# Kernel tuning notes

Hardware: AMD Instinct MI355X
Metric: run time of the kernel (lower is better)

The kernel has to match this reference:

```python
import jax, jax.numpy as jnp
import numpy as np

ALPHA = 200.0      # cfg.TRAIN.VOTING_ALPHA
RHO = 100.0        # ADMM penalty
SIGMA = 1e-3       # ADMM regularization
ITERS = 150        # fixed ADMM iterations


def _admm_qp(Q, q, C, l, u):
    n = Q.shape[0]
    K = Q + SIGMA * jnp.eye(n, dtype=Q.dtype) + RHO * (C.T @ C)
    cf = jax.scipy.linalg.cho_factor(K)
    x0 = jnp.zeros((n,), Q.dtype)
    z0 = jnp.clip(jnp.zeros((C.shape[0],), Q.dtype), l, u)
    y0 = jnp.zeros((C.shape[0],), Q.dtype)

    def step(carry, _):
        x, z, y = carry
        rhs = SIGMA * x - q + C.T @ (RHO * z - y)
        x = jax.scipy.linalg.cho_solve(cf, rhs)
        Cx = C @ x
        z = jnp.clip(Cx + y / RHO, l, u)
        y = y + RHO * (Cx - z)
        return (x, z, y), None

    (x, _, _), _ = jax.lax.scan(step, (x0, z0, y0), None, length=ITERS)
    return x


def _l2n(x, axis):
    return x / jnp.maximum(jnp.linalg.norm(x, axis=axis, keepdims=True), 1e-12)


def _forward(feat_tra, feat_det, iou_mat, W, b):
    n1, d = feat_tra.shape
    n2 = feat_det.shape[0]
    # cross-graph feature update
    Mp0 = feat_tra @ feat_det.T + iou_mat                      # (n1,n2)
    m1 = Mp0 @ feat_det                                        # (n1,d)
    m2 = Mp0.T @ feat_tra                                      # (n2,d)
    lam1 = jax.lax.stop_gradient(jnp.linalg.norm(feat_tra, axis=1, keepdims=True)
                                 / jnp.linalg.norm(m1, axis=1, keepdims=True))
    lam2 = jax.lax.stop_gradient(jnp.linalg.norm(feat_det, axis=1, keepdims=True)
                                 / jnp.linalg.norm(m2, axis=1, keepdims=True))
    e1 = jax.nn.relu((feat_tra + lam1 * m1) @ W.T + b)
    e2 = jax.nn.relu((feat_det + lam2 * m2) @ W.T + b)
    e1 = _l2n(e1, 1)
    e2 = _l2n(e2, 1)
    Mp = e1 @ e2.T                                             # (n1,n2) unary affinity
    P = Mp.T                                                   # (n2,n1)
    # Quadratic affinity: the torch code builds src_tgt[i,j,k,l] = <cat(e1_i,e1_j), cat(e2_k,e2_l)>
    # = Mp[i,k] + Mp[j,l], then gathers M[(a,c),(b,d)] = src_tgt[c,d,a,b]/2 masked by (a!=b)&(c!=d).
    ms = 1.0 - jnp.eye(n1, dtype=Mp.dtype)
    mt = 1.0 - jnp.eye(n2, dtype=Mp.dtype)
    M4 = 0.5 * (P[:, :, None, None] + P[None, None, :, :]) \
         * (mt[:, None, :, None] * ms[None, :, None, :])       # (n2,n1,n2,n1)
    n = n1 * n2
    Q = float((n1 - 1) * (n2 - 1)) * jnp.eye(n, dtype=Mp.dtype) - M4.reshape(n, n)
    q = -P.reshape(-1)                                         # -Mpp
    # equality constraints (square case): column sums and row sums == 1
    A = jnp.concatenate([jnp.kron(jnp.ones((1, n1)), jnp.eye(n2)),
                         jnp.kron(jnp.eye(n1), jnp.ones((1, n2)))], axis=0).astype(Mp.dtype)
    C = jnp.concatenate([jnp.eye(n, dtype=Mp.dtype), A], axis=0)
    l = jnp.concatenate([jnp.zeros((n,), Mp.dtype), jnp.ones((n1 + n2,), Mp.dtype)])
    u = jnp.concatenate([jnp.full((n,), 1e6, Mp.dtype), jnp.ones((n1 + n2,), Mp.dtype)])
    x = _admm_qp(Q, q, C, l, u)
    s = x.reshape(n2, n1).T                                    # (n1,n2)
    s = jnp.clip(s, 0.0, 1.0)                                  # relu(s) - relu(s-1)
    s = jax.nn.softmax(ALPHA * s, axis=-1)                     # Voting layer
    return s[None]                                             # (1,n1,n2)


def setup_inputs() -> dict:
    key = jax.random.key(0)
    k1, k2, k3, k4 = jax.random.split(key, 4)
    n1 = n2 = 64
    d = 512
    feat_tra = jax.random.normal(k1, (n1, d), jnp.float32)
    feat_det = jax.random.normal(k2, (n2, d), jnp.float32)
    iou_mat = jax.random.uniform(k3, (n1, n2), jnp.float32)
    W = jnp.eye(d, dtype=jnp.float32) + 0.01 * jax.random.normal(k4, (d, d), jnp.float32)
    b = jnp.zeros((d,), jnp.float32)
    return {"feat_tra": feat_tra, "feat_det": feat_det, "iou_mat": iou_mat, "W": W, "b": b}


def reference(feat_tra, feat_det, iou_mat, W, b):
    return _forward(feat_tra, feat_det, iou_mat, W, b)
```

## Files before the change

### kernel.cpp

```cpp
#include <hip/hip_runtime.h>
#include <math.h>

#define DD 512
#define NS 258
#define NSP 264
#define NWG 64
#define BLK 1024
#define RHO_ 100.0
#define SIG_ 1e-3
#define NITER 150
#define DELTA0 (3969.0 + SIG_ + RHO_)

typedef float v2f __attribute__((ext_vector_type(2)));

#define OFF_E1     512u
#define OFF_SUMS   512u
#define OFF_INV    4608u
#define OFF_E2     262656u
#define OFF_P      524800u
#define OFF_W      557568u
#define OFF_P32    590336u
#define OFF_W32    606720u
#define OFF_KSA    623104u
#define OFF_KSB    1168000u
#define OFF_N32    1712896u

__device__ __forceinline__ int perm258(int i){
  return (i < 128) ? i : (i == 128) ? 256 : (i == 129) ? 257 : (i - 2);
}

template<int CTRL>
__device__ __forceinline__ float dppadd(float v){
  int t = __builtin_amdgcn_mov_dpp(__float_as_int(v), CTRL, 0xF, 0xF, 1);
  return v + __int_as_float(t);
}
template<int CTRL>
__device__ __forceinline__ float dppmax(float v){
  int t = __builtin_amdgcn_mov_dpp(__float_as_int(v), CTRL, 0xF, 0xF, 1);
  return fmaxf(v, __int_as_float(t));
}
__device__ __forceinline__ float sum16(float v){
  v = dppadd<0xB1>(v);
  v = dppadd<0x4E>(v);
  v = dppadd<0x124>(v);
  v = dppadd<0x128>(v);
  return v;
}
__device__ __forceinline__ float wsum64f(float v){
  v = sum16(v);
  v += __shfl_xor(v, 16, 64);
  v += __shfl_xor(v, 32, 64);
  return v;
}
__device__ __forceinline__ float wsum64u(float v){
  v = sum16(v);
  v = dppadd<0x142>(v);
  v = dppadd<0x143>(v);
  return __uint_as_float(__builtin_amdgcn_readlane(__float_as_uint(v), 63));
}
__device__ __forceinline__ float wmax64f(float v){
  v = dppmax<0xB1>(v); v = dppmax<0x4E>(v); v = dppmax<0x124>(v); v = dppmax<0x128>(v);
  v = fmaxf(v, __shfl_xor(v, 16, 64));
  v = fmaxf(v, __shfl_xor(v, 32, 64));
  return v;
}

__device__ __forceinline__ double gsum16d(double v){
  v += __shfl_xor(v, 1, 64);
  v += __shfl_xor(v, 2, 64);
  v += __shfl_xor(v, 4, 64);
  v += __shfl_xor(v, 8, 64);
  return v;
}
__device__ __forceinline__ double wsum64d(double v){
  v = gsum16d(v);
  v += __shfl_xor(v, 16, 64);
  v += __shfl_xor(v, 32, 64);
  return v;
}

__device__ __forceinline__ void decode_idx(int t, int& cls, int& pr, int& ix){
  if (t < 64)       { cls = 1; pr = 1; ix = t; }
  else if (t < 128) { cls = 2; pr = 1; ix = t - 64; }
  else if (t == 128){ cls = 0; pr = 1; ix = 0; }
  else if (t == 129){ cls = 0; pr = 0; ix = 0; }
  else if (t < 194) { cls = 1; pr = 0; ix = t - 130; }
  else              { cls = 2; pr = 0; ix = t - 194; }
}

__device__ __forceinline__ double ksval(int r, int c, const double* __restrict__ p,
                                        const double* __restrict__ w, const double* sumsL){
  int cr, prr, ir, cc, prc, ic;
  decode_idx(r, cr, prr, ir);
  decode_idx(c, cc, prc, ic);
  int m = prr + prc;
  double tval;
  if (cr == 0 && cc == 0)      tval = sumsL[m];
  else if (cr == 0 && cc == 1) tval = sumsL[8 + m*64 + ic];
  else if (cr == 1 && cc == 0) tval = sumsL[8 + m*64 + ir];
  else if (cr == 0 && cc == 2) tval = sumsL[200 + m*64 + ic];
  else if (cr == 2 && cc == 0) tval = sumsL[200 + m*64 + ir];
  else if (cr == 1 && cc == 1) tval = (ir == ic) ? sumsL[8 + m*64 + ir] : 0.0;
  else if (cr == 2 && cc == 2) tval = (ir == ic) ? sumsL[200 + m*64 + ir] : 0.0;
  else if (cr == 1 && cc == 2){
    double wv = w[ic*64 + ir], pv = p[ic*64 + ir];
    tval = (m == 0) ? wv : (m == 1) ? wv*pv : wv*pv*pv;
  } else {
    double wv = w[ir*64 + ic], pv = p[ir*64 + ic];
    tval = (m == 0) ? wv : (m == 1) ? wv*pv : wv*pv*pv;
  }
  double mv2 = 0.0;
  if (cr == 0 && cc == 0 && prr != prc) mv2 = -2.0;
  if (cr != 0 && cr == cc && ir == ic){
    if (prr != prc) mv2 = 2.0;
    else if (prr == 1) mv2 = -4.0 * RHO_;
  }
  return tval + mv2;
}

__global__ __launch_bounds__(BLK) void kp_feat(const float* __restrict__ ft,
                                               const float* __restrict__ fd,
                                               const float* __restrict__ iou,
                                               const float* __restrict__ Wm,
                                               const float* __restrict__ bb,
                                               char* ws){
  double* e1 = (double*)(ws + OFF_E1);
  double* e2 = (double*)(ws + OFF_E2);
  __shared__ double SH[2216];
  const int tid  = threadIdx.x;
  const int wg   = blockIdx.x;
  const int lane = tid & 63;
  const int wv   = tid >> 6;
  float* ftR = (float*)SH;
  float* fdR = ftR + 512;
  float* u1R = fdR + 512;
  float* u2R = u1R + 512;
  double* m0r = SH + 1024;
  double* m0c = m0r + 64;
  double* wp  = m0c + 64;
  double* sca = wp + 32;
  double* vbuf = SH + 1192;
  const int i = wg;
  if (tid < 512){ ftR[tid] = ft[i*DD + tid]; fdR[tid] = fd[i*DD + tid]; }
  {
    double nf = 0.0, nd = 0.0;
    if (tid < 512){
      float a = ftR[tid], b = fdR[tid];
      nf = (double)a*a; nd = (double)b*b;
    }
    nf = wsum64d(nf); nd = wsum64d(nd);
    if (lane == 0){ wp[wv] = nf; wp[16 + wv] = nd; }
    __syncthreads();
    if (tid == 0){
      double s0 = 0, s1 = 0;
      for (int q = 0; q < 16; ++q){ s0 += wp[q]; s1 += wp[16+q]; }
      sca[0] = s0; sca[1] = s1;
    }
  }
  {
    int j = tid >> 4, sub = tid & 15;
    double ar = 0.0, ac = 0.0;
    for (int t2 = 0; t2 < 32; ++t2){
      int k = t2*16 + sub;
      ar += (double)ftR[k] * (double)fd[(size_t)j*DD + k];
      ac += (double)fdR[k] * (double)ft[(size_t)j*DD + k];
    }
    ar = gsum16d(ar); ac = gsum16d(ac);
    if (sub == 0){
      m0r[j] = ar + (double)iou[i*64 + j];
      m0c[j] = ac + (double)iou[j*64 + i];
    }
  }
  __syncthreads();
  {
    int c = tid & 511, half = tid >> 9;
    const double* m0 = half ? m0c : m0r;
    const float*  FB = half ? ft  : fd;
    double a0 = 0, b0 = 0, c0 = 0, d0 = 0;
    for (int a2 = 0; a2 < 64; a2 += 4){
      a0 += m0[a2]   * (double)FB[(size_t)(a2  )*DD + c];
      b0 += m0[a2+1] * (double)FB[(size_t)(a2+1)*DD + c];
      c0 += m0[a2+2] * (double)FB[(size_t)(a2+2)*DD + c];
      d0 += m0[a2+3] * (double)FB[(size_t)(a2+3)*DD + c];
    }
    double mv = (a0 + b0) + (c0 + d0);
    double nn = wsum64d(mv*mv);
    if (lane == 0) wp[wv] = nn;
    __syncthreads();
    if (tid < 2){
      double s = 0;
      for (int q = tid*8; q < tid*8 + 8; ++q) s += wp[q];
      sca[2 + tid] = sqrt(sca[tid] / s);
    }
    __syncthreads();
    double l = sca[2 + half];
    float* uR = half ? u2R : u1R;
    const float* fR = half ? fdR : ftR;
    uR[c] = (float)((double)fR[c] + l*mv);
  }
  __syncthreads();
  {
    const int g16 = tid >> 4;
    const int sub = tid & 15;
    for (int pass = 0; pass < 16; ++pass){
      int c_all = pass*64 + g16;
      int c = c_all & 511, half = c_all >> 9;
      const float* uR  = half ? u2R : u1R;
      const float* wrp = Wm + (size_t)c*DD;
      double acc = 0.0;
#pragma unroll
      for (int j = 0; j < 8; ++j){
        int k = sub*4 + j*64;
        float4 wq = *(const float4*)(wrp + k);
        float4 uq = *(const float4*)(uR + k);
        acc += (double)uq.x*wq.x + (double)uq.y*wq.y + (double)uq.z*wq.z + (double)uq.w*wq.w;
      }
      acc = gsum16d(acc);
      if (sub == 0) vbuf[c_all] = fmax(acc + (double)bb[c], 0.0);
    }
    __syncthreads();
    double v = vbuf[tid];
    double nn = wsum64d(v*v);
    if (lane == 0) wp[wv] = nn;
    __syncthreads();
    if (tid < 2){
      double s = 0;
      for (int q = tid*8; q < tid*8 + 8; ++q) s += wp[q];
      sca[4 + tid] = 1.0 / fmax(sqrt(s), 1e-12);
    }
    __syncthreads();
    int c = tid & 511, half = tid >> 9;
    double* e = half ? e2 : e1;
    e[(size_t)i*DD + c] = v * sca[4 + half];
  }
}

__global__ __launch_bounds__(BLK) void kp_pw(char* ws){
  const double* e1 = (const double*)(ws + OFF_E1);
  const double* e2 = (const double*)(ws + OFF_E2);
  double* p   = (double*)(ws + OFF_P);
  double* w   = (double*)(ws + OFF_W);
  float*  p32 = (float*) (ws + OFF_P32);
  float*  w32 = (float*) (ws + OFF_W32);
  __shared__ double e2R[512];
  const int tid = threadIdx.x;
  const int a = blockIdx.x;
  if (tid < 512) e2R[tid] = e2[(size_t)a*DD + tid];
  __syncthreads();
  int b = tid >> 4, sub = tid & 15;
  double a0 = 0.0, a1 = 0.0;
  for (int t2 = 0; t2 < 32; t2 += 2){
    a0 += e1[(size_t)b*DD + t2*16 + sub]     * e2R[t2*16 + sub];
    a1 += e1[(size_t)b*DD + (t2+1)*16 + sub] * e2R[(t2+1)*16 + sub];
  }
  double acc = gsum16d(a0 + a1);
  if (sub == 0){
    double pv = acc;
    double wv2 = 1.0 / (DELTA0 - pv);
    int jj = a*64 + b;
    p[jj] = pv; w[jj] = wv2; p32[jj] = (float)pv; w32[jj] = (float)wv2;
  }
}

__global__ __launch_bounds__(BLK) void kp_sums(char* ws){
  const double* p = (const double*)(ws + OFF_P);
  const double* w = (const double*)(ws + OFF_W);
  double* sumsG = (double*)(ws + OFF_SUMS);
  __shared__ double sumsL[456];
  const int tid = threadIdx.x;
  int a = tid >> 4, sub = tid & 15;
  {
    double r0 = 0, r1 = 0, r2 = 0;
    for (int b = sub*4; b < sub*4 + 4; ++b){
      double wv = w[a*64 + b], pv = p[a*64 + b];
      r0 += wv; r1 += wv*pv; r2 += wv*pv*pv;
    }
    r0 = gsum16d(r0); r1 = gsum16d(r1); r2 = gsum16d(r2);
    if (sub == 0){ sumsL[200 + a] = r0; sumsL[264 + a] = r1; sumsL[328 + a] = r2; }
  }
  {
    int b2 = tid >> 4;
    double c0 = 0, c1 = 0, c2 = 0;
    for (int a2 = sub*4; a2 < sub*4 + 4; ++a2){
      double wv = w[a2*64 + b2], pv = p[a2*64 + b2];
      c0 += wv; c1 += wv*pv; c2 += wv*pv*pv;
    }
    c0 = gsum16d(c0); c1 = gsum16d(c1); c2 = gsum16d(c2);
    if (sub == 0){ sumsL[8 + b2] = c0; sumsL[72 + b2] = c1; sumsL[136 + b2] = c2; }
  }
  __syncthreads();
  if (tid == 0){
    double t0 = 0, t1 = 0, t2 = 0;
    for (int a3 = 0; a3 < 64; ++a3){
      t0 += sumsL[200 + a3]; t1 += sumsL[264 + a3]; t2 += sumsL[328 + a3];
    }
    sumsL[0] = t0; sumsL[1] = t1; sumsL[2] = t2;
    sumsL[3] = 0; sumsL[4] = 0; sumsL[5] = 0; sumsL[6] = 0; sumsL[7] = 0;
  }
  if (tid >= 64 && tid < 128){
    int k = tid - 64;
    sumsL[392 + k] = 1.0 / (sumsL[136 + k] - 4.0*RHO_);
  }
  __syncthreads();
  for (int idx = tid; idx < 456; idx += BLK) sumsG[idx] = sumsL[idx];
}

__global__ __launch_bounds__(BLK) void kp_p3(char* ws){
  const double* p = (const double*)(ws + OFF_P);
  const double* w = (const double*)(ws + OFF_W);
  const double* sumsG = (const double*)(ws + OFF_SUMS);
  double* KsB = (double*)(ws + OFF_KSB);
  __shared__ double sumsL[456];
  __shared__ double temp[68];
  const int tid = threadIdx.x;
  const int c = blockIdx.x;
  for (int idx = tid; idx < 456; idx += BLK) sumsL[idx] = sumsG[idx];
  __syncthreads();
  const double* invd = sumsL + 392;
  if (tid < 64){
    int k = tid;
    temp[k] = (c < 64) ? ((k == c) ? invd[k] : 0.0) : ksval(k, c, p, w, sumsL) * invd[k];
  }
  __syncthreads();
  const double* tp = temp;
  const int s = tid & 3;
  auto dorow = [&](int rr){
    if (rr < 64){
      if (s == 0) KsB[(size_t)rr*NSP + c] = tp[rr];
      return;
    }
    double acc = 0.0;
    if (rr < 128){
      const double* wr_ = w + (rr-64)*64;
      const double* pr_ = p + (rr-64)*64;
      for (int k = s; k < 64; k += 4){ double pv = pr_[k]; acc += wr_[k]*pv*pv*tp[k]; }
    } else if (rr == 128){
      for (int k = s; k < 64; k += 4) acc += sumsL[136 + k]*tp[k];
    } else if (rr == 129){
      for (int k = s; k < 64; k += 4) acc += sumsL[72 + k]*tp[k];
    } else if (rr < 194){
      if (s == 0){ int ir = rr - 130; acc = (sumsL[72 + ir] + 2.0)*tp[ir]; }
    } else {
      int ir = rr - 194;
      const double* wr_ = w + ir*64;
      const double* pr_ = p + ir*64;
      for (int k = s; k < 64; k += 4) acc += wr_[k]*pr_[k]*tp[k];
    }
    acc += __shfl_xor(acc, 1, 64);
    acc += __shfl_xor(acc, 2, 64);
    if (s == 0){
      double first = (c < 64) ? 0.0 : ksval(rr, c, p, w, sumsL);
      KsB[(size_t)rr*NSP + c] = first - acc;
    }
  };
  { int r = tid >> 2; if (r < 256) dorow(r); }
  if (tid < 8) dorow(256 + (tid >> 2));
}

template<int MM>
__global__ __launch_bounds__(BLK) void kp_inv(const double* __restrict__ src, int p0,
                                              double* __restrict__ invG){
  __shared__ double M[MM*67];
  __shared__ double RV[MM], RV2[MM], CV[MM], CV2[MM];
  const int tid = threadIdx.x;
  const int lane = tid & 63, wv = tid >> 6;
  for (int idx = tid; idx < MM*MM; idx += BLK)
    M[(idx/MM)*67 + (idx%MM)] = src[(size_t)(p0 + idx/MM)*NSP + p0 + idx%MM];
  __syncthreads();
  for (int k = 0; k < MM; k += 2){
    if (tid < MM){
      int j = tid;
      double pk  = 1.0 / M[k*67 + k];
      double ck1 = M[(k+1)*67 + k];
      double rv  = M[k*67 + j] * pk;
      if (j == k) rv += pk;
      double rk1 = M[k*67 + k+1] * pk;
      double q   = 1.0 / (M[(k+1)*67 + k+1] - ck1*rk1);
      double r2  = (M[(k+1)*67 + j] - ck1*rv) * q;
      if (j == k+1) r2 += q;
      RV[j] = rv; RV2[j] = r2;
    } else if (tid >= 512 && tid < 512 + MM){
      int i = tid - 512;
      double pk  = 1.0 / M[k*67 + k];
      double rk1 = M[k*67 + k+1] * pk;
      double cv  = M[i*67 + k];
      if (i == k) cv -= 1.0;
      double c2  = M[i*67 + k+1] - cv*rk1;
      if (i == k+1) c2 -= 1.0;
      CV[i] = cv; CV2[i] = c2;
    }
    __syncthreads();
    {
      double rv0 = RV[lane], rv20 = RV2[lane];
      const bool hi = (lane + 64) < MM;
      double rv1 = hi ? RV[lane + 64] : 0.0;
      double rv21 = hi ? RV2[lane + 64] : 0.0;
      for (int i = wv; i < MM; i += 16){
        double cv = CV[i], c2 = CV2[i];
        M[i*67 + lane] -= cv*rv0 + c2*rv20;
        if (hi) M[i*67 + lane + 64] -= cv*rv1 + c2*rv21;
      }
    }
    __syncthreads();
  }
  for (int idx = tid; idx < MM*MM; idx += BLK)
    invG[(idx/MM)*67 + idx%MM] = M[(idx/MM)*67 + idx%MM];
}

template<int MM>
__global__ __launch_bounds__(BLK) void kp_apply(const double* __restrict__ src,
                                                double* __restrict__ dstD,
                                                float* __restrict__ dstF, int p0,
                                                const double* __restrict__ invG){
  __shared__ double M[4422];
  __shared__ double temp[68];
  __shared__ double srcMid[66];
  const int tid = threadIdx.x;
  const int c = blockIdx.x;
  for (int idx = tid; idx < MM*67; idx += BLK) M[idx] = invG[idx];
  if (tid < MM) srcMid[tid] = src[(size_t)(p0 + tid)*NSP + c];
  __syncthreads();
  const bool cpiv = (c >= p0 && c < p0 + MM);
  if (cpiv){
    if (tid < MM) temp[tid] = M[tid*67 + (c - p0)];
  } else {
    int k = tid >> 3, s8 = tid & 7;
    if (k < MM){
      double a = 0.0;
      for (int l = s8; l < MM; l += 8) a += M[k*67 + l]*srcMid[l];
      a += __shfl_xor(a, 1, 64);
      a += __shfl_xor(a, 2, 64);
      a += __shfl_xor(a, 4, 64);
      if (s8 == 0) temp[k] = a;
    }
  }
  __syncthreads();
  const int s = tid & 3;
  auto dorow = [&](int rr){
    if (rr >= p0 && rr < p0 + MM){
      if (s == 0){
        double val = temp[rr - p0];
        if (dstD) dstD[(size_t)rr*NSP + c] = val;
        else      dstF[perm258(rr)*NSP + perm258(c)] = (float)val;
      }
      return;
    }
    double acc = 0.0;
    for (int k = s; k < MM; k += 4) acc += src[(size_t)rr*NSP + p0 + k]*temp[k];
    acc += __shfl_xor(acc, 1, 64);
    acc += __shfl_xor(acc, 2, 64);
    if (s == 0){
      double f = cpiv ? 0.0 : src[(size_t)rr*NSP + c];
      double val = f - acc;
      if (dstD) dstD[(size_t)rr*NSP + c] = val;
      else      dstF[perm258(rr)*NSP + perm258(c)] = (float)val;
    }
  };
  { int r = tid >> 2; if (r < 256) dorow(r); }
  if (tid < 8) dorow(256 + (tid >> 2));
}

__global__ __launch_bounds__(BLK) __attribute__((amdgpu_waves_per_eu(4, 4)))
void k_admm(const float* __restrict__ N32,
            const float* __restrict__ p32,
            const float* __restrict__ w32,
            float* __restrict__ out){
  __shared__ float2 tb[64][66];
  __shared__ float2 csTP[64][18];
  __shared__ float  csX[64][20];
  __shared__ __align__(16) float s1f[264];
  __shared__ float s1g2[2];
  __shared__ float s2g[2];
  __shared__ __align__(16) float s2p[4][264];
  __shared__ float2 pairB[64];
  __shared__ float2 pairR[64];

  const int tid  = threadIdx.x;
  const int lane = tid & 63;
  const int wvid = tid >> 6;
  const int g    = tid >> 8;
  const int c    = tid & 255;

  float4 nc4[16];
#pragma unroll
  for (int k2 = 0; k2 < 16; ++k2){
    nc4[k2].x = N32[(64*g + 4*k2 + 0)*NSP + c];
    nc4[k2].y = N32[(64*g + 4*k2 + 1)*NSP + c];
    nc4[k2].z = N32[(64*g + 4*k2 + 2)*NSP + c];
    nc4[k2].w = N32[(64*g + 4*k2 + 3)*NSP + c];
  }
  const float ncg0 = N32[256*NSP + c];
  const float ncg1 = N32[257*NSP + c];

  float nr0 = 0.f, nr1 = 0.f, nr2 = 0.f, nr3 = 0.f, nrt0 = 0.f, nrt1 = 0.f;
  if (wvid == 4 || wvid == 5){
    int r = 252 + wvid;
    nr0 = N32[r*NSP + lane];       nr1 = N32[r*NSP + lane + 64];
    nr2 = N32[r*NSP + lane + 128]; nr3 = N32[r*NSP + lane + 192];
    nrt0 = N32[r*NSP + 256];       nrt1 = N32[r*NSP + 257];
  }

  float pr[4], wr[4], xr[4], vr[4], tq[4];
  double y2a[4], y2b = 0.0;
#pragma unroll
  for (int q = 0; q < 4; ++q){
    int j = (wvid*4 + q)*64 + lane;
    pr[q] = p32[j]; wr[q] = w32[j];
    xr[q] = 0.f; vr[q] = 0.f; tq[q] = 0.f; y2a[q] = 0.0;
  }
  __syncthreads();

  for (int it = 0; it < NITER; ++it){
    if (it){
      float ybs = 0.f;
#pragma unroll
      for (int s = 0; s < 4; ++s){
        float4 v4 = *(const float4*)&csX[lane][4*s];
        ybs += (v4.x + v4.y) + (v4.z + v4.w);
      }
      y2b += RHO_ * ((double)ybs - 1.0);
    }
    float base = (float)(2.0*RHO_ - y2b);
    float clt = 0.f, clp = 0.f;
    float st0, st1, st2, st3, sp0, sp1, sp2, sp3;
#pragma unroll
    for (int q = 0; q < 4; ++q){
      float ya = (float)y2a[q];
      float rhs = 1e-3f*xr[q] + pr[q] + 100.f*fabsf(vr[q]) + base - ya;
      float t = wr[q]*rhs;
      float pt = pr[q]*t;
      tq[q] = t;
      clt += t; clp += pt;
      float st = wsum64u(t);
      float sp = wsum64u(pt);
      if (q == 0){ st0 = st; sp0 = sp; }
      else if (q == 1){ st1 = st; sp1 = sp; }
      else if (q == 2){ st2 = st; sp2 = sp; }
      else { st3 = st; sp3 = sp; }
    }
    csTP[lane][(wvid + lane) & 15] = make_float2(clt, clp);
    {
      int l2 = lane & 3;
      float sv_ = (l2 == 0) ? st0 : (l2 == 1) ? st1 : (l2 == 2) ? st2 : st3;
      float pv_ = (l2 == 0) ? sp0 : (l2 == 1) ? sp1 : (l2 == 2) ? sp2 : sp3;
      if (lane < 4)      s1f[192 + wvid*4 + l2] = sv_;
      else if (lane < 8) s1f[64  + wvid*4 + l2] = pv_;
    }
    __syncthreads();

    if (wvid == 0){
      float ct = 0.f, cp = 0.f;
#pragma unroll
      for (int s = 0; s < 8; ++s){
        float4 v4 = *(const float4*)&csTP[lane][2*s];
        ct += v4.x + v4.z; cp += v4.y + v4.w;
      }
      s1f[128 + lane] = ct; s1f[lane] = cp;
      float tt = wsum64u(ct);
      float tp = wsum64u(cp);
      if (lane == 0){ s1g2[1] = tt; s1g2[0] = tp; }
    }
    __syncthreads();

    {
      float sv = s1f[64*g + lane];
      float a0 = 0.f, a1 = 0.f, a2 = 0.f, a3 = 0.f;
#pragma unroll
      for (int k2 = 0; k2 < 16; ++k2){
        float4 nq = nc4[k2];
        a0 += nq.x * __uint_as_float(__builtin_amdgcn_readlane(__float_as_uint(sv), 4*k2 + 0));
        a1 += nq.y * __uint_as_float(__builtin_amdgcn_readlane(__float_as_uint(sv), 4*k2 + 1));
        a2 += nq.z * __uint_as_float(__builtin_amdgcn_readlane(__float_as_uint(sv), 4*k2 + 2));
        a3 += nq.w * __uint_as_float(__builtin_amdgcn_readlane(__float_as_uint(sv), 4*k2 + 3));
      }
      float acc = (a0 + a1) + (a2 + a3);
      if (g == 0) acc += ncg0*s1g2[0] + ncg1*s1g2[1];
      s2p[g][c] = acc;
      if (wvid == 4 || wvid == 5){
        float a32 = nr0*s1f[lane] + nr1*s1f[lane+64]
                  + nr2*s1f[lane+128] + nr3*s1f[lane+192];
        a32 = wsum64u(a32);
        if (lane == 0) s2g[wvid - 4] = a32 + nrt0*s1g2[0] + nrt1*s1g2[1];
      }
    }
    __syncthreads();

    if (tid < 64){
      int b = tid;
      float sbE  = (s2p[0][128+b] + s2p[1][128+b]) + (s2p[2][128+b] + s2p[3][128+b]);
      float sbPE = (s2p[0][b] + s2p[1][b]) + (s2p[2][b] + s2p[3][b]);
      pairB[b] = make_float2(sbE, sbPE);
    } else if (tid < 128){
      int a = tid - 64;
      float sF  = (s2p[0][192+a] + s2p[1][192+a]) + (s2p[2][192+a] + s2p[3][192+a]);
      float sPF = (s2p[0][64+a] + s2p[1][64+a]) + (s2p[2][64+a] + s2p[3][64+a]);
      pairR[a] = make_float2(s2g[1] + sF, s2g[0] + sPF);
    }
    __syncthreads();

    {
      float2 pb = pairB[lane];
      float clx = 0.f;
#pragma unroll
      for (int q = 0; q < 4; ++q){
        int arow = wvid*4 + q;
        float2 prw = pairR[arow];
        float corr = prw.x + pb.x + pr[q]*(prw.y + pb.y);
        float xn = tq[q] - wr[q]*corr;
        vr[q] = xn + fminf(vr[q], 0.f);
        xr[q] = xn;
        float rsx = wsum64u(xn);
        y2a[q] += RHO_*((double)rsx - 1.0);
        clx += xn;
        if (it == NITER-1) ((float*)tb)[lane*68 + arow] = xn;
      }
      csX[lane][wvid] = clx;
    }
    __syncthreads();
  }

  const float* xb = (const float*)tb;
#pragma unroll
  for (int q = 0; q < 4; ++q){
    int i = wvid*4 + q;
    float val = xb[i*68 + lane];
    val = fminf(fmaxf(val, 0.f), 1.f);
    float mx = wmax64f(val);
    float e = expf(200.f*(val - mx));
    float sm = wsum64f(e);
    out[i*64 + lane] = e / sm;
  }
}

extern "C" void kernel_launch(void* const* d_in, const int* in_sizes, int n_in,
                              void* d_out, int out_size, void* d_ws, size_t ws_size,
                              hipStream_t stream){
  (void)in_sizes; (void)n_in; (void)out_size; (void)ws_size;
  const float* ft  = (const float*)d_in[0];
  const float* fd  = (const float*)d_in[1];
  const float* iou = (const float*)d_in[2];
  const float* Wm  = (const float*)d_in[3];
  const float* bb  = (const float*)d_in[4];
  char* ws = (char*)d_ws;

  double* KsA  = (double*)(ws + OFF_KSA);
  double* KsB  = (double*)(ws + OFF_KSB);
  double* invG = (double*)(ws + OFF_INV);
  float*  N32  = (float*) (ws + OFF_N32);

  hipLaunchKernelGGL(kp_feat, dim3(NWG), dim3(BLK), 0, stream, ft, fd, iou, Wm, bb, ws);
  hipLaunchKernelGGL(kp_pw,   dim3(NWG), dim3(BLK), 0, stream, ws);
  hipLaunchKernelGGL(kp_sums, dim3(1),   dim3(BLK), 0, stream, ws);
  hipLaunchKernelGGL(kp_p3,   dim3(NS),  dim3(BLK), 0, stream, ws);

  hipLaunchKernelGGL(kp_inv<66>,   dim3(1),  dim3(BLK), 0, stream, KsB, 64, invG);
  hipLaunchKernelGGL(kp_apply<66>, dim3(NS), dim3(BLK), 0, stream, KsB, KsA, (float*)nullptr, 64, invG);
  hipLaunchKernelGGL(kp_inv<64>,   dim3(1),  dim3(BLK), 0, stream, KsA, 130, invG);
  hipLaunchKernelGGL(kp_apply<64>, dim3(NS), dim3(BLK), 0, stream, KsA, KsB, (float*)nullptr, 130, invG);
  hipLaunchKernelGGL(kp_inv<64>,   dim3(1),  dim3(BLK), 0, stream, KsB, 194, invG);
  hipLaunchKernelGGL(kp_apply<64>, dim3(NS), dim3(BLK), 0, stream, KsB, (double*)nullptr, N32, 194, invG);

  const float* p32 = (const float*)(ws + OFF_P32);
  const float* w32 = (const float*)(ws + OFF_W32);
  hipLaunchKernelGGL(k_admm, dim3(1), dim3(BLK), 0, stream, N32, p32, w32, (float*)d_out);
}
```

Baseline: 689.9 us.

## Block kp_inv elimination four pivots per pass and drop ADMM pair-reduction barrier

The Gauss-Jordan inversion kernel now eliminates four pivots per round instead of two. It builds the third and fourth pivot row and column vectors from the first two before applying one combined rank-4 update, which halves the number of shared-memory update sweeps and barriers. In the ADMM iteration loop, the separate pairB/pairR reduction stage and its barrier are removed. Every wave now redundantly sums the four s2p partials it needs. This trades extra shared-memory loads and arithmetic for fewer synchronizations per iteration.

```diff
diff --git a/kernel.cpp b/kernel.cpp
--- a/kernel.cpp
+++ b/kernel.cpp
@@ -361,13 +361,15 @@
 __global__ __launch_bounds__(BLK) void kp_inv(const double* __restrict__ src, int p0,
                                               double* __restrict__ invG){
   __shared__ double M[MM*67];
-  __shared__ double RV[MM], RV2[MM], CV[MM], CV2[MM];
+  __shared__ double RV1[MM], RV2[MM], RV3[MM], RV4[MM];
+  __shared__ double CV1[MM], CV2[MM], CV3[MM], CV4[MM];
   const int tid = threadIdx.x;
   const int lane = tid & 63, wv = tid >> 6;
   for (int idx = tid; idx < MM*MM; idx += BLK)
     M[(idx/MM)*67 + (idx%MM)] = src[(size_t)(p0 + idx/MM)*NSP + p0 + idx%MM];
   __syncthreads();
-  for (int k = 0; k < MM; k += 2){
+  constexpr int K4 = (MM/4)*4;
+  for (int k = 0; k < K4; k += 4){
     if (tid < MM){
       int j = tid;
       double pk  = 1.0 / M[k*67 + k];
@@ -378,7 +380,7 @@
       double q   = 1.0 / (M[(k+1)*67 + k+1] - ck1*rk1);
       double r2  = (M[(k+1)*67 + j] - ck1*rv) * q;
       if (j == k+1) r2 += q;
-      RV[j] = rv; RV2[j] = r2;
+      RV1[j] = rv; RV2[j] = r2;
     } else if (tid >= 512 && tid < 512 + MM){
       int i = tid - 512;
       double pk  = 1.0 / M[k*67 + k];
@@ -387,18 +389,88 @@
       if (i == k) cv -= 1.0;
       double c2  = M[i*67 + k+1] - cv*rk1;
       if (i == k+1) c2 -= 1.0;
-      CV[i] = cv; CV2[i] = c2;
+      CV1[i] = cv; CV2[i] = c2;
     }
     __syncthreads();
     {
-      double rv0 = RV[lane], rv20 = RV2[lane];
+      const int a = k+2, b = k+3;
+      if (tid < MM){
+        int j = tid;
+        double cv1a = CV1[a], cv2a = CV2[a], cv1b = CV1[b], cv2b = CV2[b];
+        double rv1a = RV1[a], rv2a = RV2[a], rv1b = RV1[b], rv2b = RV2[b];
+        double pk3 = 1.0 / (M[a*67 + a] - cv1a*rv1a - cv2a*rv2a);
+        double ck3 = M[b*67 + a] - cv1b*rv1a - cv2b*rv2a;
+        double m_aj = M[a*67 + j] - cv1a*RV1[j] - cv2a*RV2[j];
+        double rv3 = m_aj * pk3;
+        if (j == a) rv3 += pk3;
+        double rk3 = (M[a*67 + b] - cv1a*rv1b - cv2a*rv2b) * pk3;
+        double Mbb = M[b*67 + b] - cv1b*rv1b - cv2b*rv2b;
+        double q3 = 1.0 / (Mbb - ck3*rk3);
+        double m_bj = M[b*67 + j] - cv1b*RV1[j] - cv2b*RV2[j];
+        double rv4 = (m_bj - ck3*rv3) * q3;
+        if (j == b) rv4 += q3;
+        RV3[j] = rv3; RV4[j] = rv4;
+      } else if (tid >= 512 && tid < 512 + MM){
+        int i = tid - 512;
+        double cv1a = CV1[a], cv2a = CV2[a];
+        double rv1a = RV1[a], rv2a = RV2[a], rv1b = RV1[b], rv2b = RV2[b];
+        double pk3 = 1.0 / (M[a*67 + a] - cv1a*rv1a - cv2a*rv2a);
+        double rk3 = (M[a*67 + b] - cv1a*rv1b - cv2a*rv2b) * pk3;
+        double cv1i = CV1[i], cv2i = CV2[i];
+        double cv3 = M[i*67 + a] - cv1i*rv1a - cv2i*rv2a;
+        if (i == a) cv3 -= 1.0;
+        double m_ib = M[i*67 + b] - cv1i*rv1b - cv2i*rv2b;
+        double cv4 = m_ib - cv3*rk3;
+        if (i == b) cv4 -= 1.0;
+        CV3[i] = cv3; CV4[i] = cv4;
+      }
+    }
+    __syncthreads();
+    {
+      double r1l = RV1[lane], r2l = RV2[lane], r3l = RV3[lane], r4l = RV4[lane];
       const bool hi = (lane + 64) < MM;
-      double rv1 = hi ? RV[lane + 64] : 0.0;
-      double rv21 = hi ? RV2[lane + 64] : 0.0;
+      double r1h = hi ? RV1[lane+64] : 0.0, r2h = hi ? RV2[lane+64] : 0.0;
+      double r3h = hi ? RV3[lane+64] : 0.0, r4h = hi ? RV4[lane+64] : 0.0;
       for (int i = wv; i < MM; i += 16){
-        double cv = CV[i], c2 = CV2[i];
-        M[i*67 + lane] -= cv*rv0 + c2*rv20;
-        if (hi) M[i*67 + lane + 64] -= cv*rv1 + c2*rv21;
+        double c1 = CV1[i], c2 = CV2[i], c3 = CV3[i], c4 = CV4[i];
+        M[i*67 + lane] -= (c1*r1l + c2*r2l) + (c3*r3l + c4*r4l);
+        if (hi) M[i*67 + lane + 64] -= (c1*r1h + c2*r2h) + (c3*r3h + c4*r4h);
+      }
+    }
+    __syncthreads();
+  }
+  if constexpr (K4 < MM){
+    const int k = K4;
+    if (tid < MM){
+      int j = tid;
+      double pk  = 1.0 / M[k*67 + k];
+      double ck1 = M[(k+1)*67 + k];
+      double rv  = M[k*67 + j] * pk;
+      if (j == k) rv += pk;
+      double rk1 = M[k*67 + k+1] * pk;
+      double q   = 1.0 / (M[(k+1)*67 + k+1] - ck1*rk1);
+      double r2  = (M[(k+1)*67 + j] - ck1*rv) * q;
+      if (j == k+1) r2 += q;
+      RV1[j] = rv; RV2[j] = r2;
+    } else if (tid >= 512 && tid < 512 + MM){
+      int i = tid - 512;
+      double pk  = 1.0 / M[k*67 + k];
+      double rk1 = M[k*67 + k+1] * pk;
+      double cv  = M[i*67 + k];
+      if (i == k) cv -= 1.0;
+      double c2  = M[i*67 + k+1] - cv*rk1;
+      if (i == k+1) c2 -= 1.0;
+      CV1[i] = cv; CV2[i] = c2;
+    }
+    __syncthreads();
+    {
+      double r1l = RV1[lane], r2l = RV2[lane];
+      const bool hi = (lane + 64) < MM;
+      double r1h = hi ? RV1[lane+64] : 0.0, r2h = hi ? RV2[lane+64] : 0.0;
+      for (int i = wv; i < MM; i += 16){
+        double c1 = CV1[i], c2 = CV2[i];
+        M[i*67 + lane] -= c1*r1l + c2*r2l;
+        if (hi) M[i*67 + lane + 64] -= c1*r1h + c2*r2h;
       }
     }
     __syncthreads();
@@ -472,8 +544,6 @@
   __shared__ float s1g2[2];
   __shared__ float s2g[2];
   __shared__ __align__(16) float s2p[4][264];
-  __shared__ float2 pairB[64];
-  __shared__ float2 pairR[64];
 
   const int tid  = threadIdx.x;
   const int lane = tid & 63;
@@ -585,27 +655,17 @@
     }
     __syncthreads();
 
-    if (tid < 64){
-      int b = tid;
-      float sbE  = (s2p[0][128+b] + s2p[1][128+b]) + (s2p[2][128+b] + s2p[3][128+b]);
-      float sbPE = (s2p[0][b] + s2p[1][b]) + (s2p[2][b] + s2p[3][b]);
-      pairB[b] = make_float2(sbE, sbPE);
-    } else if (tid < 128){
-      int a = tid - 64;
-      float sF  = (s2p[0][192+a] + s2p[1][192+a]) + (s2p[2][192+a] + s2p[3][192+a]);
-      float sPF = (s2p[0][64+a] + s2p[1][64+a]) + (s2p[2][64+a] + s2p[3][64+a]);
-      pairR[a] = make_float2(s2g[1] + sF, s2g[0] + sPF);
-    }
-    __syncthreads();
-
     {
-      float2 pb = pairB[lane];
+      float sbE  = (s2p[0][128+lane] + s2p[1][128+lane]) + (s2p[2][128+lane] + s2p[3][128+lane]);
+      float sbPE = (s2p[0][lane] + s2p[1][lane]) + (s2p[2][lane] + s2p[3][lane]);
+      float g1 = s2g[1], g0 = s2g[0];
       float clx = 0.f;
 #pragma unroll
       for (int q = 0; q < 4; ++q){
         int arow = wvid*4 + q;
-        float2 prw = pairR[arow];
-        float corr = prw.x + pb.x + pr[q]*(prw.y + pb.y);
+        float sF  = (s2p[0][192+arow] + s2p[1][192+arow]) + (s2p[2][192+arow] + s2p[3][192+arow]);
+        float sPF = (s2p[0][64+arow] + s2p[1][64+arow]) + (s2p[2][64+arow] + s2p[3][64+arow]);
+        float corr = (g1 + sF) + sbE + pr[q]*((g0 + sPF) + sbPE);
         float xn = tq[q] - wr[q]*corr;
         vr[q] = xn + fminf(vr[q], 0.f);
         xr[q] = xn;
```

Measured after the change: 706.1 us. 1.02x slower.
